# Optimization experiments

Hardware: AMD Instinct MI355X
Metric: run time of the kernel (lower is better)

Reference implementation:

```python
import jax, jax.numpy as jnp
import numpy as np

N, E, G = 4096, 16384, 16
IN_C, EDGE_C, H = 3, 4, 128
LN_EPS = 1e-5


def setup_inputs() -> dict:
    key = jax.random.key(0)
    ks = jax.random.split(key, 32)
    nrm = lambda k, shp, s: jax.random.normal(k, shp, jnp.float32) * s
    inp = {}
    inp["x"] = nrm(ks[0], (N, IN_C), 1.0)
    inp["edge_index"] = jax.random.randint(ks[1], (2, E), 0, N)
    inp["edge_attr"] = nrm(ks[2], (E, EDGE_C), 1.0)
    inp["batch"] = jnp.sort(jax.random.randint(ks[3], (N,), 0, G))
    inp["contingency_type"] = nrm(ks[4], (G, 4), 1.0)
    inp["load_scale"] = nrm(ks[5], (G,), 1.0)
    i = 6
    def conv_params(prefix, in_c):
        nonlocal i
        inp[prefix + "_w1"] = nrm(ks[i], (EDGE_C, 128), 1.0 / np.sqrt(EDGE_C)); i += 1
        inp[prefix + "_b1"] = jnp.zeros((128,), jnp.float32)
        inp[prefix + "_w2"] = nrm(ks[i], (128, in_c * H), 1.0 / np.sqrt(128)); i += 1
        inp[prefix + "_b2"] = jnp.zeros((in_c * H,), jnp.float32)
        inp[prefix + "_root"] = nrm(ks[i], (in_c, H), 1.0 / np.sqrt(in_c)); i += 1
        inp[prefix + "_bias"] = jnp.zeros((H,), jnp.float32)
    conv_params("c1", IN_C)
    conv_params("c2", H)
    conv_params("c3", H)
    for p in ("ln1", "ln2", "ln3"):
        inp[p + "_g"] = jnp.ones((H,), jnp.float32)
        inp[p + "_b"] = jnp.zeros((H,), jnp.float32)
    inp["lin_w"] = nrm(ks[i], (2 * H + 4 + 1, 2), 1.0 / np.sqrt(2 * H + 5)); i += 1
    inp["lin_b"] = jnp.zeros((2,), jnp.float32)
    return inp


def _nnconv(x, src, dst, edge_attr, w1, b1, w2, b2, root, bias, in_c):
    # edge MLP -> per-edge weight matrix [E, in_c, H]
    h = jax.nn.relu(edge_attr @ w1 + b1)
    W = (h @ w2 + b2).reshape(-1, in_c, H)
    msg = jnp.einsum('ei,eio->eo', x[src], W)  # gather + per-edge matmul
    s = jax.ops.segment_sum(msg, dst, num_segments=N)
    cnt = jax.ops.segment_sum(jnp.ones((msg.shape[0],), msg.dtype), dst, num_segments=N)
    agg = s / jnp.maximum(cnt, 1.0)[:, None]  # scatter-mean
    return agg + x @ root + bias


def _layernorm(x, g, b):
    m = jnp.mean(x, axis=-1, keepdims=True)
    v = jnp.mean(jnp.square(x - m), axis=-1, keepdims=True)
    return (x - m) * jax.lax.rsqrt(v + LN_EPS) * g + b


def reference(x, edge_index, edge_attr, batch, contingency_type, load_scale,
              c1_w1, c1_b1, c1_w2, c1_b2, c1_root, c1_bias,
              c2_w1, c2_b1, c2_w2, c2_b2, c2_root, c2_bias,
              c3_w1, c3_b1, c3_w2, c3_b2, c3_root, c3_bias,
              ln1_g, ln1_b, ln2_g, ln2_b, ln3_g, ln3_b,
              lin_w, lin_b):
    src, dst = edge_index[0], edge_index[1]
    h = _nnconv(x, src, dst, edge_attr, c1_w1, c1_b1, c1_w2, c1_b2, c1_root, c1_bias, IN_C)
    h = jax.nn.relu(_layernorm(h, ln1_g, ln1_b))
    h = _nnconv(h, src, dst, edge_attr, c2_w1, c2_b1, c2_w2, c2_b2, c2_root, c2_bias, H)
    h = jax.nn.elu(_layernorm(h, ln2_g, ln2_b))
    h = _nnconv(h, src, dst, edge_attr, c3_w1, c3_b1, c3_w2, c3_b2, c3_root, c3_bias, H)
    h = jax.nn.leaky_relu(_layernorm(h, ln3_g, ln3_b), negative_slope=0.01)
    # global mean / max pool over graphs
    gsum = jax.ops.segment_sum(h, batch, num_segments=G)
    gcnt = jax.ops.segment_sum(jnp.ones((N,), h.dtype), batch, num_segments=G)
    gmean = gsum / jnp.maximum(gcnt, 1.0)[:, None]
    gmax = jax.ops.segment_max(h, batch, num_segments=G)
    gmax = jnp.where(gcnt[:, None] > 0, gmax, 0.0)
    x_cat = jnp.concatenate([gmean, gmax, contingency_type, load_scale[:, None]], axis=1)
    return x_cat @ lin_w + lin_b
```

## Files before the change

kernel.cpp:

```cpp
#include <hip/hip_runtime.h>
#include <hip/hip_bf16.h>


#define N_NODES 4096
#define N_EDGES 16384
#define N_GRAPHS 16
#define HD 128
#define BM 128
#define LDB 136
#define KSPLIT 2
#define KT_PER (HD / KSPLIT)
#define SLAB_E (HD * HD)

typedef unsigned short ushort_t;
typedef __attribute__((ext_vector_type(8))) short short8;
typedef __attribute__((ext_vector_type(4))) float f32x4;

static __device__ __forceinline__ ushort_t f2b(float f) {
    __hip_bfloat16 h = __float2bfloat16(f);
    union { __hip_bfloat16 h; ushort_t u; } cv; cv.h = h; return cv.u;
}
static __device__ __forceinline__ float b2f(ushort_t u) {
    union { unsigned u; float f; } cv; cv.u = ((unsigned)u) << 16; return cv.f;
}

static __device__ __forceinline__ float wave_sum(float v) {
#pragma unroll
    for (int off = 1; off < 64; off <<= 1) v += __shfl_xor(v, off, 64);
    return v;
}

__global__ __launch_bounds__(256) void count_k(const int* __restrict__ dst, float* __restrict__ cnt) {
    int e = blockIdx.x * 256 + threadIdx.x;
    atomicAdd(&cnt[dst[e]], 1.0f);
}

__global__ __launch_bounds__(128) void l1_edge(
    const float* __restrict__ x, const int* __restrict__ src, const int* __restrict__ dst,
    const float* __restrict__ ea, const float* __restrict__ w1, const float* __restrict__ b1,
    const float* __restrict__ w2, const float* __restrict__ b2, float* __restrict__ agg) {
    __shared__ float h[4][HD];
    __shared__ float xsrc[4][3];
    const int o = threadIdx.x;
    const int e0 = blockIdx.x * 4;
#pragma unroll
    for (int q = 0; q < 4; ++q) {
        float s = b1[o];
#pragma unroll
        for (int j = 0; j < 4; ++j) s = fmaf(ea[(e0 + q) * 4 + j], w1[j * HD + o], s);
        h[q][o] = fmaxf(s, 0.0f);
    }
    if (o < 12) { int q = o / 3, i = o % 3; xsrc[q][i] = x[src[e0 + q] * 3 + i]; }
    __syncthreads();
    float acc[4] = {0.f, 0.f, 0.f, 0.f};
    for (int i = 0; i < 3; ++i) {
        float bb = b2[i * HD + o];
        float w[4] = {bb, bb, bb, bb};
        for (int k = 0; k < HD; ++k) {
            float w2v = w2[k * 384 + i * HD + o];
#pragma unroll
            for (int q = 0; q < 4; ++q) w[q] = fmaf(h[q][k], w2v, w[q]);
        }
#pragma unroll
        for (int q = 0; q < 4; ++q) acc[q] = fmaf(xsrc[q][i], w[q], acc[q]);
    }
#pragma unroll
    for (int q = 0; q < 4; ++q) atomicAdd(&agg[dst[e0 + q] * HD + o], acc[q]);
}

__global__ __launch_bounds__(128) void node_update_l1(
    float* __restrict__ agg, const float* __restrict__ cnt, const float* __restrict__ x,
    const float* __restrict__ root, const float* __restrict__ bias,
    const float* __restrict__ lng, const float* __restrict__ lnb) {
    const int n = blockIdx.x, o = threadIdx.x;
    float s = bias[o];
#pragma unroll
    for (int i = 0; i < 3; ++i) s = fmaf(x[n * 3 + i], root[i * HD + o], s);
    float v = agg[n * HD + o] / fmaxf(cnt[n], 1.0f) + s;
    __shared__ float red[2];
    float ws = wave_sum(v);
    if ((o & 63) == 0) red[o >> 6] = ws;
    __syncthreads();
    float m = (red[0] + red[1]) * (1.0f / HD);
    float d = v - m;
    float ws2 = wave_sum(d * d);
    __syncthreads();
    if ((o & 63) == 0) red[o >> 6] = ws2;
    __syncthreads();
    float var = (red[0] + red[1]) * (1.0f / HD);
    float y = d * rsqrtf(var + 1e-5f) * lng[o] + lnb[o];
    agg[n * HD + o] = fmaxf(y, 0.0f);
}

__global__ __launch_bounds__(256) void w2t_prep(const float* __restrict__ w2,
                                                const float* __restrict__ b2,
                                                ushort_t* __restrict__ w2t) {
    __shared__ ushort_t tile[HD][LDB];
    const int kt = blockIdx.x;
    const int t = threadIdx.x;
    const float* srcp = (kt < HD) ? (w2 + kt * HD * HD) : b2;
    for (int c = 0; c < 64; ++c) {
        int flat = c * 256 + t;
        int i = flat >> 7, o = flat & 127;
        tile[o][i] = f2b(srcp[i * HD + o]);
    }
    __syncthreads();
    uint4* outp = (uint4*)(w2t + kt * HD * HD);
    for (int c = 0; c < 8; ++c) {
        int f = c * 256 + t;
        int o = f >> 4, i0 = (f & 15) * 8;
        outp[f] = *(const uint4*)&tile[o][i0];
    }
}

__global__ __launch_bounds__(512, 2) void gemm_mfma(
    const float* __restrict__ hprev, const float* __restrict__ ea,
    const float* __restrict__ w1, const float* __restrict__ b1,
    const ushort_t* __restrict__ w2t,
    const int* __restrict__ src, const int* __restrict__ dst,
    float* __restrict__ agg) {
    __shared__ ushort_t Bs[3 * SLAB_E];
    __shared__ ushort_t HeT[KT_PER + 1][BM];

    const int t = threadIdx.x;
    const int wave = t >> 6, lane = t & 63;
    const int quad = lane >> 4, l16 = lane & 15;
    const int mg = wave >> 2;
    const int ng = wave & 3;
    const int eb = blockIdx.x >> 1;
    const int ks = blockIdx.x & 1;
    const int k0 = ks * KT_PER;
    const int e0 = eb * BM;
    const int rbase = mg * 64;
    const int n0 = ng * 32;
    const int nslab = ks ? (KT_PER + 1) : KT_PER;

#define GSLAB(s) (((s) < KT_PER) ? (k0 + (s)) : HD)
#define ASMBAR  { asm volatile("s_waitcnt lgkmcnt(0)" ::: "memory"); \
                  __builtin_amdgcn_s_barrier(); }

#define LOADG(va, vb, vc, vd, kt)                                               \
    {                                                                           \
        const uint4* gp = (const uint4*)(w2t + (size_t)(kt) * SLAB_E);          \
        va = gp[t]; vb = gp[t + 512]; vc = gp[t + 1024]; vd = gp[t + 1536];     \
    }
    const int dr0 = t >> 4;
    const int dswoff = dr0 * HD + (((t & 15) ^ (dr0 & 7)) << 3);
#define DSW(wp, va, vb, vc, vd)                                                 \
    {                                                                           \
        *(uint4*)((wp) + dswoff)         = va;                                  \
        *(uint4*)((wp) + dswoff + 4096)  = vb;                                  \
        *(uint4*)((wp) + dswoff + 8192)  = vc;                                  \
        *(uint4*)((wp) + dswoff + 12288) = vd;                                  \
    }
#define READF(bf, bp)                                                           \
    {                                                                           \
        _Pragma("unroll") for (int ni = 0; ni < 2; ++ni) {                      \
            const int R = n0 + ni * 16 + l16;                                   \
            const ushort_t* rowp = (bp) + R * HD;                               \
            const int r7 = R & 7;                                               \
            _Pragma("unroll") for (int kb = 0; kb < 4; ++kb)                    \
                bf[ni][kb] = *(const short8*)&rowp[((kb * 4 + quad) ^ r7) << 3];\
        }                                                                       \
    }
#define CONSUME(bf, s)                                                          \
    {                                                                           \
        _Pragma("unroll") for (int mi = 0; mi < 4; ++mi) {                      \
            ushort4 hv = *(const ushort4*)&HeT[s][rbase + mi * 16 + quad * 4];  \
            float h0 = b2f(hv.x), h1 = b2f(hv.y), h2 = b2f(hv.z), h3 = b2f(hv.w);\
            _Pragma("unroll") for (int ni = 0; ni < 2; ++ni) {                  \
                f32x4 p = {0.f, 0.f, 0.f, 0.f};                                 \
                _Pragma("unroll") for (int kb = 0; kb < 4; ++kb)                \
                    p = __builtin_amdgcn_mfma_f32_16x16x32_bf16(                \
                        afrag[mi][kb], bf[ni][kb], p, 0, 0, 0);                 \
                acc[mi][ni][0] = fmaf(h0, p[0], acc[mi][ni][0]);                \
                acc[mi][ni][1] = fmaf(h1, p[1], acc[mi][ni][1]);                \
                acc[mi][ni][2] = fmaf(h2, p[2], acc[mi][ni][2]);                \
                acc[mi][ni][3] = fmaf(h3, p[3], acc[mi][ni][3]);                \
            }                                                                   \
        }                                                                       \
    }

    uint4 s0a, s0b, s0c, s0d, s1a, s1b, s1c, s1d;
    LOADG(s0a, s0b, s0c, s0d, GSLAB(0));
    LOADG(s1a, s1b, s1c, s1d, GSLAB(1));

    {
        const int le = t >> 2;
        const int j0 = (t & 3) * 4;
        const int r7 = le & 7;
        const float* rp = hprev + src[e0 + le] * HD + (t & 3) * 32;
        ushort_t* xrow = Bs + 2 * SLAB_E + le * HD;
#pragma unroll
        for (int c = 0; c < 4; ++c) {
            float4 va = ((const float4*)rp)[2 * c];
            float4 vb = ((const float4*)rp)[2 * c + 1];
            uint4 pk;
            pk.x = (unsigned)f2b(va.x) | ((unsigned)f2b(va.y) << 16);
            pk.y = (unsigned)f2b(va.z) | ((unsigned)f2b(va.w) << 16);
            pk.z = (unsigned)f2b(vb.x) | ((unsigned)f2b(vb.y) << 16);
            pk.w = (unsigned)f2b(vb.z) | ((unsigned)f2b(vb.w) << 16);
            *(uint4*)&xrow[((j0 + c) ^ r7) << 3] = pk;
        }
    }

    {
        const int e = t & 127;
        const float4 av = ((const float4*)ea)[e0 + e];
        const float a0 = av.x, a1 = av.y, a2 = av.z, a3 = av.w;
        for (int kl = t >> 7; kl < KT_PER; kl += 4) {
            const int kt = k0 + kl;
            float s = b1[kt];
            s = fmaf(a0, w1[0 * HD + kt], s);
            s = fmaf(a1, w1[1 * HD + kt], s);
            s = fmaf(a2, w1[2 * HD + kt], s);
            s = fmaf(a3, w1[3 * HD + kt], s);
            HeT[kl][e] = f2b(fmaxf(s, 0.0f));
        }
        if (ks == 1 && (t >> 7) == 0) HeT[KT_PER][e] = f2b(1.0f);
    }
    ASMBAR;

    short8 afrag[4][4];
    {
        const ushort_t* xp = Bs + 2 * SLAB_E;
#pragma unroll
        for (int mi = 0; mi < 4; ++mi) {
            const int R = rbase + mi * 16 + l16;
            const ushort_t* rowp = xp + R * HD;
            const int r7 = R & 7;
#pragma unroll
            for (int kb = 0; kb < 4; ++kb)
                afrag[mi][kb] = *(const short8*)&rowp[((kb * 4 + quad) ^ r7) << 3];
        }
    }

    DSW(Bs, s0a, s0b, s0c, s0d);
    LOADG(s0a, s0b, s0c, s0d, GSLAB(2));
    DSW(Bs + SLAB_E, s1a, s1b, s1c, s1d);
    LOADG(s1a, s1b, s1c, s1d, GSLAB(3));

    f32x4 acc[4][2];
#pragma unroll
    for (int mi = 0; mi < 4; ++mi)
#pragma unroll
        for (int ni = 0; ni < 2; ++ni)
            acc[mi][ni] = (f32x4){0.f, 0.f, 0.f, 0.f};

    ASMBAR;

    short8 bf[2][4];
    unsigned bsel = 0;
    for (int s = 0; s < KT_PER; s += 2) {
        {
            ushort_t* bp = Bs + bsel * SLAB_E;
            unsigned wsel = bsel + 2; if (wsel >= 3) wsel -= 3;
            READF(bf, bp);
            if (s + 2 < nslab) { ushort_t* wp = Bs + wsel * SLAB_E; DSW(wp, s0a, s0b, s0c, s0d); }
            if (s + 4 < nslab) LOADG(s0a, s0b, s0c, s0d, GSLAB(s + 4));
            CONSUME(bf, s);
            ASMBAR;
            bsel = (bsel >= 2) ? 0 : bsel + 1;
        }
        {
            ushort_t* bp = Bs + bsel * SLAB_E;
            unsigned wsel = bsel + 2; if (wsel >= 3) wsel -= 3;
            READF(bf, bp);
            if (s + 3 < nslab) { ushort_t* wp = Bs + wsel * SLAB_E; DSW(wp, s1a, s1b, s1c, s1d); }
            if (s + 5 < nslab) LOADG(s1a, s1b, s1c, s1d, GSLAB(s + 5));
            CONSUME(bf, s + 1);
            ASMBAR;
            bsel = (bsel >= 2) ? 0 : bsel + 1;
        }
    }
    if (nslab > KT_PER) {
        ushort_t* bp = Bs + bsel * SLAB_E;
        READF(bf, bp);
        CONSUME(bf, KT_PER);
    }
#undef GSLAB
#undef ASMBAR
#undef LOADG
#undef DSW
#undef READF
#undef CONSUME

#pragma unroll
    for (int mi = 0; mi < 4; ++mi) {
#pragma unroll
        for (int r = 0; r < 4; ++r) {
            const int dn = dst[e0 + rbase + mi * 16 + quad * 4 + r];
#pragma unroll
            for (int ni = 0; ni < 2; ++ni)
                atomicAdd(&agg[dn * HD + n0 + ni * 16 + l16], acc[mi][ni][r]);
        }
    }
}

__global__ __launch_bounds__(128) void node_update(
    float* __restrict__ agg, const float* __restrict__ cnt,
    const float* __restrict__ hprev, const float* __restrict__ root, const float* __restrict__ bias,
    const float* __restrict__ lng, const float* __restrict__ lnb, int act) {
    const int n = blockIdx.x, o = threadIdx.x;
    __shared__ float hr[HD];
    hr[o] = hprev[n * HD + o];
    __syncthreads();
    float s = bias[o];
#pragma unroll 8
    for (int k = 0; k < HD; ++k) s = fmaf(hr[k], root[k * HD + o], s);
    float v = agg[n * HD + o] / fmaxf(cnt[n], 1.0f) + s;
    __shared__ float red[2];
    float ws = wave_sum(v);
    if ((o & 63) == 0) red[o >> 6] = ws;
    __syncthreads();
    float m = (red[0] + red[1]) * (1.0f / HD);
    float d = v - m;
    float ws2 = wave_sum(d * d);
    __syncthreads();
    if ((o & 63) == 0) red[o >> 6] = ws2;
    __syncthreads();
    float var = (red[0] + red[1]) * (1.0f / HD);
    float y = d * rsqrtf(var + 1e-5f) * lng[o] + lnb[o];
    if (act == 1) y = (y > 0.0f) ? y : expm1f(y);
    else y = (y > 0.0f) ? y : 0.01f * y;
    agg[n * HD + o] = y;
}

static __device__ __forceinline__ unsigned fkey(float f) {
    unsigned b = __float_as_uint(f);
    return (b & 0x80000000u) ? ~b : (b | 0x80000000u);
}
__global__ __launch_bounds__(256) void pool_scatter(
    const float* __restrict__ h3, const int* __restrict__ batch,
    float* __restrict__ gsum, unsigned* __restrict__ gmaxk, int* __restrict__ gcnt) {
    const int idx = blockIdx.x * 256 + threadIdx.x;
    const int n = idx >> 7, o = idx & 127;
    const int g = batch[n];
    const float v = h3[idx];
    atomicAdd(&gsum[g * HD + o], v);
    atomicMax(&gmaxk[g * HD + o], fkey(v));
    if (o == 0) atomicAdd(&gcnt[g], 1);
}

__global__ __launch_bounds__(128) void pool_head2(
    const float* __restrict__ gsum, const unsigned* __restrict__ gmaxk, const int* __restrict__ gcnt,
    const float* __restrict__ cont, const float* __restrict__ ls,
    const float* __restrict__ lin_w, const float* __restrict__ lin_b, float* __restrict__ out) {
    const int g = blockIdx.x, o = threadIdx.x;
    const int c = gcnt[g];
    __shared__ float xcat[2 * HD + 5];
    xcat[o] = gsum[g * HD + o] / fmaxf((float)c, 1.0f);
    unsigned key = gmaxk[g * HD + o];
    unsigned bits = (key & 0x80000000u) ? (key & 0x7FFFFFFFu) : ~key;
    xcat[HD + o] = (c > 0) ? __uint_as_float(bits) : 0.0f;
    if (o < 4) xcat[2 * HD + o] = cont[g * 4 + o];
    if (o == 0) xcat[2 * HD + 4] = ls[g];
    __syncthreads();
    if (o < 2) {
        float r = lin_b[o];
        for (int ri = 0; ri < 2 * HD + 5; ++ri) r = fmaf(xcat[ri], lin_w[ri * 2 + o], r);
        out[g * 2 + o] = r;
    }
}

extern "C" void kernel_launch(void* const* d_in, const int* in_sizes, int n_in,
                              void* d_out, int out_size, void* d_ws, size_t ws_size,
                              hipStream_t stream) {
    const float* x     = (const float*)d_in[0];
    const int*   ei    = (const int*)d_in[1];
    const float* ea    = (const float*)d_in[2];
    const int*   batch = (const int*)d_in[3];
    const float* cont  = (const float*)d_in[4];
    const float* ls    = (const float*)d_in[5];
    const float *c1_w1 = (const float*)d_in[6],  *c1_b1 = (const float*)d_in[7];
    const float *c1_w2 = (const float*)d_in[8],  *c1_b2 = (const float*)d_in[9];
    const float *c1_rt = (const float*)d_in[10], *c1_bs = (const float*)d_in[11];
    const float *c2_w1 = (const float*)d_in[12], *c2_b1 = (const float*)d_in[13];
    const float *c2_w2 = (const float*)d_in[14], *c2_b2 = (const float*)d_in[15];
    const float *c2_rt = (const float*)d_in[16], *c2_bs = (const float*)d_in[17];
    const float *c3_w1 = (const float*)d_in[18], *c3_b1 = (const float*)d_in[19];
    const float *c3_w2 = (const float*)d_in[20], *c3_b2 = (const float*)d_in[21];
    const float *c3_rt = (const float*)d_in[22], *c3_bs = (const float*)d_in[23];
    const float *ln1g = (const float*)d_in[24], *ln1b = (const float*)d_in[25];
    const float *ln2g = (const float*)d_in[26], *ln2b = (const float*)d_in[27];
    const float *ln3g = (const float*)d_in[28], *ln3b = (const float*)d_in[29];
    const float *lin_w = (const float*)d_in[30], *lin_b = (const float*)d_in[31];
    float* out = (float*)d_out;

    float*    cnt  = (float*)d_ws;
    float*    bufA = cnt + N_NODES;
    float*    bufB = bufA + N_NODES * HD;
    ushort_t* w2t  = (ushort_t*)(bufB + N_NODES * HD);
    float*    gsum = (float*)(w2t + (HD + 1) * HD * HD);
    unsigned* gmaxk = (unsigned*)(gsum + N_GRAPHS * HD);
    int*      gcnt = (int*)(gmaxk + N_GRAPHS * HD);
    const int* src = ei;
    const int* dst = ei + N_EDGES;

    hipMemsetAsync(cnt, 0, N_NODES * sizeof(float), stream);
    count_k<<<N_EDGES / 256, 256, 0, stream>>>(dst, cnt);

    hipMemsetAsync(bufA, 0, N_NODES * HD * sizeof(float), stream);
    l1_edge<<<N_EDGES / 4, 128, 0, stream>>>(x, src, dst, ea, c1_w1, c1_b1, c1_w2, c1_b2, bufA);
    node_update_l1<<<N_NODES, 128, 0, stream>>>(bufA, cnt, x, c1_rt, c1_bs, ln1g, ln1b);

    w2t_prep<<<HD + 1, 256, 0, stream>>>(c2_w2, c2_b2, w2t);
    hipMemsetAsync(bufB, 0, N_NODES * HD * sizeof(float), stream);
    gemm_mfma<<<(N_EDGES / BM) * KSPLIT, 512, 0, stream>>>(bufA, ea, c2_w1, c2_b1, w2t, src, dst, bufB);
    node_update<<<N_NODES, 128, 0, stream>>>(bufB, cnt, bufA, c2_rt, c2_bs, ln2g, ln2b, 1);

    w2t_prep<<<HD + 1, 256, 0, stream>>>(c3_w2, c3_b2, w2t);
    hipMemsetAsync(bufA, 0, N_NODES * HD * sizeof(float), stream);
    gemm_mfma<<<(N_EDGES / BM) * KSPLIT, 512, 0, stream>>>(bufB, ea, c3_w1, c3_b1, w2t, src, dst, bufA);
    node_update<<<N_NODES, 128, 0, stream>>>(bufA, cnt, bufB, c3_rt, c3_bs, ln3g, ln3b, 2);

    hipMemsetAsync(gsum, 0, (2 * N_GRAPHS * HD + N_GRAPHS) * sizeof(float), stream);
    pool_scatter<<<N_NODES * HD / 256, 256, 0, stream>>>(bufA, batch, gsum, gmaxk, gcnt);
    pool_head2<<<N_GRAPHS, 128, 0, stream>>>(gsum, gmaxk, gcnt, cont, ls, lin_w, lin_b, out);
}
```

Measured before the change: 432.6 us.

## Use four LDS slabs to halve GEMM barriers and pre-reduce pooling atomics

The edge GEMM moves from a three-slab rotating buffer to four slabs. Each loop iteration now consumes two k-slabs back to back and then hits a single barrier, so there are half as many barriers. The cost is more LDS use, which could limit occupancy. Global pooling now has each thread run-length reduce sum and max over 32 sorted nodes before issuing atomics, which replaces one atomic per element.

```diff
diff --git a/kernel.cpp b/kernel.cpp
--- a/kernel.cpp
+++ b/kernel.cpp
@@ -11,6 +11,7 @@
 #define KSPLIT 2
 #define KT_PER (HD / KSPLIT)
 #define SLAB_E (HD * HD)
+#define PN 32
 
 typedef unsigned short ushort_t;
 typedef __attribute__((ext_vector_type(8))) short short8;
@@ -119,7 +120,7 @@
     const ushort_t* __restrict__ w2t,
     const int* __restrict__ src, const int* __restrict__ dst,
     float* __restrict__ agg) {
-    __shared__ ushort_t Bs[3 * SLAB_E];
+    __shared__ ushort_t Bs[4 * SLAB_E];
     __shared__ ushort_t HeT[KT_PER + 1][BM];
 
     const int t = threadIdx.x;
@@ -190,7 +191,7 @@
         const int j0 = (t & 3) * 4;
         const int r7 = le & 7;
         const float* rp = hprev + src[e0 + le] * HD + (t & 3) * 32;
-        ushort_t* xrow = Bs + 2 * SLAB_E + le * HD;
+        ushort_t* xrow = Bs + 3 * (size_t)SLAB_E + le * HD;
 #pragma unroll
         for (int c = 0; c < 4; ++c) {
             float4 va = ((const float4*)rp)[2 * c];
@@ -223,7 +224,7 @@
 
     short8 afrag[4][4];
     {
-        const ushort_t* xp = Bs + 2 * SLAB_E;
+        const ushort_t* xp = Bs + 3 * (size_t)SLAB_E;
 #pragma unroll
         for (int mi = 0; mi < 4; ++mi) {
             const int R = rbase + mi * 16 + l16;
@@ -236,8 +237,8 @@
     }
 
     DSW(Bs, s0a, s0b, s0c, s0d);
+    DSW(Bs + SLAB_E, s1a, s1b, s1c, s1d);
     LOADG(s0a, s0b, s0c, s0d, GSLAB(2));
-    DSW(Bs + SLAB_E, s1a, s1b, s1c, s1d);
     LOADG(s1a, s1b, s1c, s1d, GSLAB(3));
 
     f32x4 acc[4][2];
@@ -249,34 +250,24 @@
 
     ASMBAR;
 
-    short8 bf[2][4];
-    unsigned bsel = 0;
+    short8 bf0[2][4], bf1[2][4];
     for (int s = 0; s < KT_PER; s += 2) {
-        {
-            ushort_t* bp = Bs + bsel * SLAB_E;
-            unsigned wsel = bsel + 2; if (wsel >= 3) wsel -= 3;
-            READF(bf, bp);
-            if (s + 2 < nslab) { ushort_t* wp = Bs + wsel * SLAB_E; DSW(wp, s0a, s0b, s0c, s0d); }
-            if (s + 4 < nslab) LOADG(s0a, s0b, s0c, s0d, GSLAB(s + 4));
-            CONSUME(bf, s);
-            ASMBAR;
-            bsel = (bsel >= 2) ? 0 : bsel + 1;
-        }
-        {
-            ushort_t* bp = Bs + bsel * SLAB_E;
-            unsigned wsel = bsel + 2; if (wsel >= 3) wsel -= 3;
-            READF(bf, bp);
-            if (s + 3 < nslab) { ushort_t* wp = Bs + wsel * SLAB_E; DSW(wp, s1a, s1b, s1c, s1d); }
-            if (s + 5 < nslab) LOADG(s1a, s1b, s1c, s1d, GSLAB(s + 5));
-            CONSUME(bf, s + 1);
-            ASMBAR;
-            bsel = (bsel >= 2) ? 0 : bsel + 1;
-        }
+        ushort_t* bpe = Bs + (size_t)(s & 3) * SLAB_E;
+        ushort_t* bpo = Bs + (size_t)((s + 1) & 3) * SLAB_E;
+        READF(bf0, bpe);
+        CONSUME(bf0, s);
+        if (s + 2 < nslab) { ushort_t* wp = Bs + (size_t)((s + 2) & 3) * SLAB_E; DSW(wp, s0a, s0b, s0c, s0d); }
+        if (s + 3 < nslab) { ushort_t* wp = Bs + (size_t)((s + 3) & 3) * SLAB_E; DSW(wp, s1a, s1b, s1c, s1d); }
+        if (s + 4 < nslab) LOADG(s0a, s0b, s0c, s0d, GSLAB(s + 4));
+        if (s + 5 < nslab) LOADG(s1a, s1b, s1c, s1d, GSLAB(s + 5));
+        READF(bf1, bpo);
+        CONSUME(bf1, s + 1);
+        ASMBAR;
     }
     if (nslab > KT_PER) {
-        ushort_t* bp = Bs + bsel * SLAB_E;
-        READF(bf, bp);
-        CONSUME(bf, KT_PER);
+        ushort_t* bp = Bs + (size_t)(KT_PER & 3) * SLAB_E;
+        READF(bf0, bp);
+        CONSUME(bf0, KT_PER);
     }
 #undef GSLAB
 #undef ASMBAR
@@ -330,16 +321,29 @@
     unsigned b = __float_as_uint(f);
     return (b & 0x80000000u) ? ~b : (b | 0x80000000u);
 }
-__global__ __launch_bounds__(256) void pool_scatter(
+__global__ __launch_bounds__(128) void pool_scatter(
     const float* __restrict__ h3, const int* __restrict__ batch,
     float* __restrict__ gsum, unsigned* __restrict__ gmaxk, int* __restrict__ gcnt) {
-    const int idx = blockIdx.x * 256 + threadIdx.x;
-    const int n = idx >> 7, o = idx & 127;
-    const int g = batch[n];
-    const float v = h3[idx];
-    atomicAdd(&gsum[g * HD + o], v);
-    atomicMax(&gmaxk[g * HD + o], fkey(v));
-    if (o == 0) atomicAdd(&gcnt[g], 1);
+    const int o = threadIdx.x;
+    const int nb = blockIdx.x * PN;
+    float sum = 0.0f, mx = -3.0e38f;
+    int gcur = batch[nb];
+    int run = 0;
+    for (int j = 0; j < PN; ++j) {
+        const int n = nb + j;
+        const int g = batch[n];
+        const float v = h3[n * HD + o];
+        if (g != gcur) {
+            atomicAdd(&gsum[gcur * HD + o], sum);
+            atomicMax(&gmaxk[gcur * HD + o], fkey(mx));
+            if (o == 0) atomicAdd(&gcnt[gcur], run);
+            sum = 0.0f; mx = -3.0e38f; run = 0; gcur = g;
+        }
+        sum += v; mx = fmaxf(mx, v); ++run;
+    }
+    atomicAdd(&gsum[gcur * HD + o], sum);
+    atomicMax(&gmaxk[gcur * HD + o], fkey(mx));
+    if (o == 0) atomicAdd(&gcnt[gcur], run);
 }
 
 __global__ __launch_bounds__(128) void pool_head2(
@@ -415,6 +419,6 @@
     node_update<<<N_NODES, 128, 0, stream>>>(bufA, cnt, bufB, c3_rt, c3_bs, ln3g, ln3b, 2);
 
     hipMemsetAsync(gsum, 0, (2 * N_GRAPHS * HD + N_GRAPHS) * sizeof(float), stream);
-    pool_scatter<<<N_NODES * HD / 256, 256, 0, stream>>>(bufA, batch, gsum, gmaxk, gcnt);
+    pool_scatter<<<N_NODES / PN, 128, 0, stream>>>(bufA, batch, gsum, gmaxk, gcnt);
     pool_head2<<<N_GRAPHS, 128, 0, stream>>>(gsum, gmaxk, gcnt, cont, ls, lin_w, lin_b, out);
 }
```

Measured after the change: 388.0 us. -10.3%, faster.
